# Kernel optimization log

Measured on AMD Instinct MI355X. Metric: run time of the kernel, lower is better.

The kernel has to match this reference:

```python
import jax, jax.numpy as jnp
from jax import lax
import numpy as np

DIM = 64
NUM_HEADS = 1
SR_RATIO = 8
LN_EPS = 1e-3  # Keras LayerNormalization default


def setup_inputs() -> dict:
    key = jax.random.key(0)
    ks = jax.random.split(key, 8)
    B, H, W = 8, 128, 128
    N, C = H * W, DIM
    s = 0.02
    x = jax.random.normal(ks[0], (B, N, C), dtype=jnp.float32)
    Wq = jax.random.normal(ks[1], (C, C), dtype=jnp.float32) * s
    Wkv = jax.random.normal(ks[2], (C, 2 * C), dtype=jnp.float32) * s
    sr_kernel = jax.random.normal(ks[3], (SR_RATIO, SR_RATIO, C, C), dtype=jnp.float32) * s
    sr_bias = jnp.zeros((C,), dtype=jnp.float32)
    ln_gamma = jnp.ones((C,), dtype=jnp.float32)
    ln_beta = jnp.zeros((C,), dtype=jnp.float32)
    Wproj = jax.random.normal(ks[4], (C, C), dtype=jnp.float32) * s
    bproj = jnp.zeros((C,), dtype=jnp.float32)
    return {"x": x, "H": H, "W": W, "Wq": Wq, "Wkv": Wkv,
            "sr_kernel": sr_kernel, "sr_bias": sr_bias,
            "ln_gamma": ln_gamma, "ln_beta": ln_beta,
            "Wproj": Wproj, "bproj": bproj}


def reference(x, H, W, Wq, Wkv, sr_kernel, sr_bias, ln_gamma, ln_beta, Wproj, bproj):
    B, N, C = x.shape
    nh = NUM_HEADS
    hd = C // nh
    scale = hd ** -0.5

    # q: [B, nh, N, hd]
    q = (x @ Wq).reshape(B, N, nh, hd).transpose(0, 2, 1, 3)

    # spatial-reduction KV path (faithful to the TF code, incl. its
    # transpose-then-reshape ordering)
    x_ = jnp.transpose(x, (0, 2, 1)).reshape(B, H, W, C)
    x_ = lax.conv_general_dilated(
        x_, sr_kernel, window_strides=(SR_RATIO, SR_RATIO), padding="VALID",
        dimension_numbers=("NHWC", "HWIO", "NHWC")) + sr_bias
    M = x_.shape[1] * x_.shape[2]
    x_ = x_.reshape(B, M, C)
    # LayerNorm over last axis
    mu = jnp.mean(x_, axis=-1, keepdims=True)
    var = jnp.mean(jnp.square(x_ - mu), axis=-1, keepdims=True)
    x_ = (x_ - mu) * lax.rsqrt(var + LN_EPS) * ln_gamma + ln_beta

    kv = (x_ @ Wkv).reshape(B, M, 2, nh, hd).transpose(2, 0, 3, 1, 4)
    k, v = kv[0], kv[1]  # [B, nh, M, hd]

    attn = jax.nn.softmax(jnp.einsum("bhnd,bhmd->bhnm", q, k) * scale, axis=-1)
    out = jnp.einsum("bhnm,bhmd->bhnd", attn, v)
    out = out.transpose(0, 2, 1, 3).reshape(B, N, C)
    return out @ Wproj + bproj
```

## Files before the change

### kernel.cpp

```cpp
#include <hip/hip_runtime.h>
#include <hip/hip_bf16.h>

#define B_   8
#define N_   16384
#define C_   64
#define M_   256
#define NPB  1048576

typedef __attribute__((ext_vector_type(8))) short short8v;
typedef __attribute__((ext_vector_type(16))) float f32x16;
typedef __attribute__((ext_vector_type(4)))  float f32x4;

union FragU { short8v s8; unsigned u[4]; };

__device__ inline unsigned pkbf(float a, float b) {
  union { __hip_bfloat162 h2; unsigned u; } cv;
  cv.h2 = __float22bfloat162_rn(make_float2(a, b));
  return cv.u;
}
__device__ inline unsigned short bfbits(float a) {
  union { __hip_bfloat16 h; unsigned short u; } cv;
  cv.h = __float2bfloat16(a);
  return cv.u;
}
__device__ inline float bf2f(unsigned short u) {
  union { unsigned u; float f; } cv;
  cv.u = ((unsigned)u) << 16;
  return cv.f;
}
__device__ inline short8v ld8(const unsigned short* p) {
  return *(const short8v*)p;
}

__device__ inline void plswap(unsigned &a, unsigned &b) {
#if __has_builtin(__builtin_amdgcn_permlane32_swap)
  typedef unsigned uint2v __attribute__((ext_vector_type(2)));
  uint2v r = __builtin_amdgcn_permlane32_swap(a, b, false, false);
  a = r[0]; b = r[1];
#else
  asm volatile("v_permlane32_swap_b32 %0, %1" : "+v"(a), "+v"(b));
#endif
}

__device__ inline void repack16(const f32x16 s, FragU& f0, FragU& f1) {
  #pragma unroll
  for (int h = 0; h < 2; ++h) {
    FragU& f = h ? f1 : f0;
    unsigned a0 = pkbf(s[8*h+0], s[8*h+1]);
    unsigned a1 = pkbf(s[8*h+2], s[8*h+3]);
    unsigned a2 = pkbf(s[8*h+4], s[8*h+5]);
    unsigned a3 = pkbf(s[8*h+6], s[8*h+7]);
    plswap(a0, a2);
    plswap(a1, a3);
    f.u[0] = a0; f.u[1] = a1; f.u[2] = a2; f.u[3] = a3;
  }
}

__global__ __launch_bounds__(256) void prep(const float* __restrict__ Wq,
                                            const float* __restrict__ Wp,
                                            const float* __restrict__ Kw,
                                            const float* __restrict__ Wkv,
                                            unsigned short* __restrict__ kbt,
                                            float* __restrict__ wkp,
                                            float* __restrict__ wvp) {
  const int gi = blockIdx.x;
  if (gi < 1024) {
    const int idx = gi * 256 + threadIdx.x;
    const int j = idx & 7, l = (idx >> 3) & 63, s = (idx >> 9) & 15;
    const int w = (idx >> 13) & 3, kw = idx >> 15;
    const int e = s * 32 + 8 * (l >> 4) + j;
    const int par = e >> 8, ci = (e >> 2) & 63, jj = e & 3;
    const int kh = 2 * jj + par, co = 16 * w + (l & 15);
    kbt[idx] = bfbits(Kw[(size_t)((kh * 8 + kw) * 64 + ci) * 64 + co]);
  } else {
    const int idx = (gi - 1024) * 256 + threadIdx.x;
    const int c = idx & 63, cc = (idx >> 6) & 63, sel = idx >> 12;
    float s = 0.f;
    if (sel == 0) {
      #pragma unroll 8
      for (int d = 0; d < 64; ++d) s += Wkv[cc * 128 + d] * Wq[c * 64 + d];
      wkp[cc * 64 + c] = s * 0.125f;
    } else {
      #pragma unroll 8
      for (int d = 0; d < 64; ++d) s += Wkv[cc * 128 + 64 + d] * Wp[d * 64 + c];
      wvp[cc * 64 + c] = s;
    }
  }
}

__global__ __launch_bounds__(256) void conv_mfma(const float* __restrict__ x,
                                                 const unsigned short* __restrict__ kbt,
                                                 unsigned short* __restrict__ xrb) {
  const int kw = blockIdx.x & 7;
  const int ow = (blockIdx.x >> 3) & 15;
  const int b  = blockIdx.x >> 7;
  const int t  = threadIdx.x, w = t >> 6, l = t & 63;
  const int oh = l & 15, kg = l >> 4;

  const float* xb = x + (size_t)b * NPB + (size_t)((ow * 8 + kw) * 64) * 64 + oh * 4;
  const unsigned short* kb = kbt + (size_t)(((kw * 4 + w) * 16) * 64 + l) * 8;

  f32x4 acc = {0.f, 0.f, 0.f, 0.f};
  #pragma unroll
  for (int s = 0; s < 16; ++s) {
    const int par = (s >= 8) ? 1 : 0;
    const int ci  = ((s * 8) + kg * 2) & 63;
    const float* ax = xb + (size_t)par * 524288 + ci * 64;
    const float4 a0 = *(const float4*)(ax);
    const float4 a1 = *(const float4*)(ax + 64);
    FragU af;
    af.u[0] = pkbf(a0.x, a0.y); af.u[1] = pkbf(a0.z, a0.w);
    af.u[2] = pkbf(a1.x, a1.y); af.u[3] = pkbf(a1.z, a1.w);
    const short8v bfrag = ld8(kb + s * 512);
    acc = __builtin_amdgcn_mfma_f32_16x16x32_bf16(af.s8, bfrag, acc, 0, 0, 0);
  }
  unsigned short* dst = xrb + (size_t)kw * 131072
                      + ((size_t)b * 256 + ow) * 64 + w * 16 + (l & 15);
  #pragma unroll
  for (int r = 0; r < 4; ++r)
    dst[(size_t)((l >> 4) * 4 + r) * 1024] = bfbits(acc[r]);
}

__global__ __launch_bounds__(256) void ln_kv(const unsigned short* __restrict__ xrb,
                                             const float* __restrict__ sr_bias,
                                             const float* __restrict__ gamma,
                                             const float* __restrict__ beta,
                                             const float* __restrict__ wkp,
                                             const float* __restrict__ wvp,
                                             unsigned short* __restrict__ kbl,
                                             unsigned short* __restrict__ vbl) {
  const int w   = threadIdx.x >> 6;
  const int row = blockIdx.x * 4 + w;
  const int c   = threadIdx.x & 63;
  float val = sr_bias[c];
  #pragma unroll
  for (int s = 0; s < 8; ++s)
    val += bf2f(xrb[(size_t)s * 131072 + (size_t)row * 64 + c]);

  float sum = val;
  #pragma unroll
  for (int off = 32; off; off >>= 1) sum += __shfl_xor(sum, off, 64);
  const float mu = sum * (1.f / 64.f);
  const float d  = val - mu;
  float vs = d * d;
  #pragma unroll
  for (int off = 32; off; off >>= 1) vs += __shfl_xor(vs, off, 64);
  const float rs = rsqrtf(vs * (1.f / 64.f) + 1e-3f);
  const float ln = d * rs * gamma[c] + beta[c];

  __shared__ float lnrow[4][64];
  lnrow[w][c] = ln;
  __syncthreads();

  float ka = 0.f, va = 0.f;
  #pragma unroll 8
  for (int cc = 0; cc < 64; ++cc) {
    const float l = lnrow[w][cc];
    ka += l * wkp[cc * 64 + c];
    va += l * wvp[cc * 64 + c];
  }
  const int m = row & 255, bb = row >> 8;
  kbl[(size_t)bb * 16384
      + (size_t)((((m >> 5) * 4 + (c >> 4)) * 64) + (m & 31) + 32 * ((c >> 3) & 1)) * 8
      + (c & 7)] = bfbits(ka);
  vbl[(size_t)bb * 16384
      + (size_t)(((c >> 5) * 8 + (m >> 5)) * 2 + ((m >> 4) & 1)) * 512
      + (size_t)((c & 31) + 32 * ((m >> 3) & 1)) * 8
      + (m & 7)] = bfbits(va);
}

__global__ __launch_bounds__(256, 4) void attn_mfma(const float* __restrict__ x,
                                                    const unsigned short* __restrict__ kbl,
                                                    const unsigned short* __restrict__ vbl,
                                                    const float* __restrict__ bp,
                                                    float* __restrict__ out) {
  __shared__ float ot[128 * 68];
  const int t    = threadIdx.x;
  const int w    = t >> 6;
  const int l    = t & 63;
  const int l31  = l & 31;
  const int hi   = l >> 5;
  const int b    = blockIdx.x >> 7;
  const int tile = blockIdx.x & 127;
  const size_t nrow = (size_t)b * N_ + (size_t)tile * 128;
  const int qrow = w * 32 + l31;

  const float* xrow = x + (nrow + qrow) * 64;
  FragU xb[4];
  #pragma unroll
  for (int tt = 0; tt < 4; ++tt) {
    const float* p = xrow + 16 * tt + 8 * hi;
    const float4 x0 = *(const float4*)(p);
    const float4 x1 = *(const float4*)(p + 4);
    xb[tt].u[0] = pkbf(x0.x, x0.y); xb[tt].u[1] = pkbf(x0.z, x0.w);
    xb[tt].u[2] = pkbf(x1.x, x1.y); xb[tt].u[3] = pkbf(x1.z, x1.w);
  }

  const unsigned short* kfp = kbl + (size_t)b * 16384 + l * 8;
  const unsigned short* vfp = vbl + (size_t)b * 16384 + l * 8;
  f32x16 O0, O1;
  #pragma unroll
  for (int r = 0; r < 16; ++r) { O0[r] = 0.f; O1[r] = 0.f; }
  float ss = 0.f;

  #pragma unroll
  for (int kt = 0; kt < 8; ++kt) {
    const short8v vf00 = ld8(vfp + (size_t)((kt * 2 + 0) * 512));
    const short8v vf01 = ld8(vfp + (size_t)((kt * 2 + 1) * 512));
    const short8v vf10 = ld8(vfp + (size_t)(((8 + kt) * 2 + 0) * 512));
    const short8v vf11 = ld8(vfp + (size_t)(((8 + kt) * 2 + 1) * 512));
    f32x16 S;
    #pragma unroll
    for (int r = 0; r < 16; ++r) S[r] = 0.f;
    #pragma unroll
    for (int tt = 0; tt < 4; ++tt) {
      const short8v ak = ld8(kfp + (size_t)((kt * 4 + tt) * 512));
      S = __builtin_amdgcn_mfma_f32_32x32x16_bf16(ak, xb[tt].s8, S, 0, 0, 0);
    }
    f32x16 P;
    #pragma unroll
    for (int r = 0; r < 16; ++r) {
      const float pv = __expf(S[r]);
      P[r] = pv; ss += pv;
    }
    FragU f0, f1;
    repack16(P, f0, f1);
    O0 = __builtin_amdgcn_mfma_f32_32x32x16_bf16(vf00, f0.s8, O0, 0, 0, 0);
    O0 = __builtin_amdgcn_mfma_f32_32x32x16_bf16(vf01, f1.s8, O0, 0, 0, 0);
    O1 = __builtin_amdgcn_mfma_f32_32x32x16_bf16(vf10, f0.s8, O1, 0, 0, 0);
    O1 = __builtin_amdgcn_mfma_f32_32x32x16_bf16(vf11, f1.s8, O1, 0, 0, 0);
  }

  ss += __shfl_xor(ss, 32);
  const float inv = 1.f / ss;
  #pragma unroll
  for (int g = 0; g < 4; ++g) {
    {
      const int co = 8 * g + 4 * hi;
      const float4 bb = *(const float4*)(bp + co);
      *(float4*)&ot[qrow * 68 + co] =
          make_float4(O0[4 * g + 0] * inv + bb.x, O0[4 * g + 1] * inv + bb.y,
                      O0[4 * g + 2] * inv + bb.z, O0[4 * g + 3] * inv + bb.w);
    }
    {
      const int co = 32 + 8 * g + 4 * hi;
      const float4 bb = *(const float4*)(bp + co);
      *(float4*)&ot[qrow * 68 + co] =
          make_float4(O1[4 * g + 0] * inv + bb.x, O1[4 * g + 1] * inv + bb.y,
                      O1[4 * g + 2] * inv + bb.z, O1[4 * g + 3] * inv + bb.w);
    }
  }

  __syncthreads();
  float4* out4 = (float4*)(out + nrow * 64);
  #pragma unroll
  for (int i = 0; i < 8; ++i) {
    const int idx = i * 256 + t;
    const int row = idx >> 4, c4 = idx & 15;
    out4[idx] = *(const float4*)&ot[row * 68 + c4 * 4];
  }
}

extern "C" void kernel_launch(void* const* d_in, const int* in_sizes, int n_in,
                              void* d_out, int out_size, void* d_ws, size_t ws_size,
                              hipStream_t stream) {
  const float* x   = (const float*)d_in[0];
  const float* Wq  = (const float*)d_in[3];
  const float* Wkv = (const float*)d_in[4];
  const float* Kw  = (const float*)d_in[5];
  const float* sb  = (const float*)d_in[6];
  const float* gam = (const float*)d_in[7];
  const float* bet = (const float*)d_in[8];
  const float* Wp  = (const float*)d_in[9];
  const float* bp  = (const float*)d_in[10];
  float* out = (float*)d_out;

  unsigned short* xrb = (unsigned short*)d_ws;
  unsigned short* kbl = xrb + 1048576;
  unsigned short* vbl = kbl + 131072;
  unsigned short* kbt = vbl + 131072;
  float* wkp = (float*)(kbt + 262144);
  float* wvp = wkp + 4096;

  prep<<<1056, 256, 0, stream>>>(Wq, Wp, Kw, Wkv, kbt, wkp, wvp);
  conv_mfma<<<1024, 256, 0, stream>>>(x, kbt, xrb);
  ln_kv<<<512, 256, 0, stream>>>(xrb, sb, gam, bet, wkp, wvp, kbl, vbl);
  attn_mfma<<<1024, 256, 0, stream>>>(x, kbl, vbl, bp, out);
}
```

Before: 46.85 us.

## Process two query tiles per wave to reuse K/V fragments, use exp2

Each wave of the attention kernel now handles 64 query rows as two 32-row sub-tiles, so every loaded K and V fragment feeds twice as many MFMAs and the block count halves. The log2(e) factor is folded into the precomputed key weight so softmax can use exp2f instead of __expf. Launch bounds drop to 2 blocks per CU to make room for the doubled accumulator registers, and the output is written in two passes through the same shared tile with extra barriers. The cost is fewer resident waves per CU and more synchronisation in the epilogue.

```diff
diff --git a/kernel.cpp b/kernel.cpp
--- a/kernel.cpp
+++ b/kernel.cpp
@@ -79,7 +79,7 @@
     if (sel == 0) {
       #pragma unroll 8
       for (int d = 0; d < 64; ++d) s += Wkv[cc * 128 + d] * Wq[c * 64 + d];
-      wkp[cc * 64 + c] = s * 0.125f;
+      wkp[cc * 64 + c] = s * 0.125f * 1.4426950408889634f;
     } else {
       #pragma unroll 8
       for (int d = 0; d < 64; ++d) s += Wkv[cc * 128 + 64 + d] * Wp[d * 64 + c];
@@ -169,7 +169,7 @@
       + (m & 7)] = bfbits(va);
 }
 
-__global__ __launch_bounds__(256, 4) void attn_mfma(const float* __restrict__ x,
+__global__ __launch_bounds__(256, 2) void attn_mfma(const float* __restrict__ x,
                                                     const unsigned short* __restrict__ kbl,
                                                     const unsigned short* __restrict__ vbl,
                                                     const float* __restrict__ bp,
@@ -180,28 +180,34 @@
   const int l    = t & 63;
   const int l31  = l & 31;
   const int hi   = l >> 5;
-  const int b    = blockIdx.x >> 7;
-  const int tile = blockIdx.x & 127;
-  const size_t nrow = (size_t)b * N_ + (size_t)tile * 128;
-  const int qrow = w * 32 + l31;
-
-  const float* xrow = x + (nrow + qrow) * 64;
-  FragU xb[4];
+  const int b    = blockIdx.x >> 6;
+  const int tile = blockIdx.x & 63;
+  const size_t nrow = (size_t)b * N_ + (size_t)tile * 256;
+  const int qA = w * 64 + l31;
+
+  const float* xrowA = x + (nrow + qA) * 64;
+  FragU xa[4], xbb[4];
   #pragma unroll
   for (int tt = 0; tt < 4; ++tt) {
-    const float* p = xrow + 16 * tt + 8 * hi;
-    const float4 x0 = *(const float4*)(p);
-    const float4 x1 = *(const float4*)(p + 4);
-    xb[tt].u[0] = pkbf(x0.x, x0.y); xb[tt].u[1] = pkbf(x0.z, x0.w);
-    xb[tt].u[2] = pkbf(x1.x, x1.y); xb[tt].u[3] = pkbf(x1.z, x1.w);
+    const float* pA = xrowA + 16 * tt + 8 * hi;
+    const float4 a0 = *(const float4*)(pA);
+    const float4 a1 = *(const float4*)(pA + 4);
+    xa[tt].u[0] = pkbf(a0.x, a0.y); xa[tt].u[1] = pkbf(a0.z, a0.w);
+    xa[tt].u[2] = pkbf(a1.x, a1.y); xa[tt].u[3] = pkbf(a1.z, a1.w);
+    const float* pB = pA + 32 * 64;
+    const float4 b0 = *(const float4*)(pB);
+    const float4 b1 = *(const float4*)(pB + 4);
+    xbb[tt].u[0] = pkbf(b0.x, b0.y); xbb[tt].u[1] = pkbf(b0.z, b0.w);
+    xbb[tt].u[2] = pkbf(b1.x, b1.y); xbb[tt].u[3] = pkbf(b1.z, b1.w);
   }
 
   const unsigned short* kfp = kbl + (size_t)b * 16384 + l * 8;
   const unsigned short* vfp = vbl + (size_t)b * 16384 + l * 8;
-  f32x16 O0, O1;
-  #pragma unroll
-  for (int r = 0; r < 16; ++r) { O0[r] = 0.f; O1[r] = 0.f; }
-  float ss = 0.f;
+  f32x16 Z;
+  #pragma unroll
+  for (int r = 0; r < 16; ++r) Z[r] = 0.f;
+  f32x16 OA0 = Z, OA1 = Z, OB0 = Z, OB1 = Z;
+  float ssA = 0.f, ssB = 0.f;
 
   #pragma unroll
   for (int kt = 0; kt < 8; ++kt) {
@@ -209,55 +215,88 @@
     const short8v vf01 = ld8(vfp + (size_t)((kt * 2 + 1) * 512));
     const short8v vf10 = ld8(vfp + (size_t)(((8 + kt) * 2 + 0) * 512));
     const short8v vf11 = ld8(vfp + (size_t)(((8 + kt) * 2 + 1) * 512));
-    f32x16 S;
-    #pragma unroll
-    for (int r = 0; r < 16; ++r) S[r] = 0.f;
-    #pragma unroll
-    for (int tt = 0; tt < 4; ++tt) {
-      const short8v ak = ld8(kfp + (size_t)((kt * 4 + tt) * 512));
-      S = __builtin_amdgcn_mfma_f32_32x32x16_bf16(ak, xb[tt].s8, S, 0, 0, 0);
-    }
-    f32x16 P;
+    const short8v ak0 = ld8(kfp + (size_t)((kt * 4 + 0) * 512));
+    const short8v ak1 = ld8(kfp + (size_t)((kt * 4 + 1) * 512));
+    const short8v ak2 = ld8(kfp + (size_t)((kt * 4 + 2) * 512));
+    const short8v ak3 = ld8(kfp + (size_t)((kt * 4 + 3) * 512));
+    f32x16 Sa = __builtin_amdgcn_mfma_f32_32x32x16_bf16(ak0, xa[0].s8, Z, 0, 0, 0);
+    f32x16 Sb = __builtin_amdgcn_mfma_f32_32x32x16_bf16(ak0, xbb[0].s8, Z, 0, 0, 0);
+    Sa = __builtin_amdgcn_mfma_f32_32x32x16_bf16(ak1, xa[1].s8, Sa, 0, 0, 0);
+    Sb = __builtin_amdgcn_mfma_f32_32x32x16_bf16(ak1, xbb[1].s8, Sb, 0, 0, 0);
+    Sa = __builtin_amdgcn_mfma_f32_32x32x16_bf16(ak2, xa[2].s8, Sa, 0, 0, 0);
+    Sb = __builtin_amdgcn_mfma_f32_32x32x16_bf16(ak2, xbb[2].s8, Sb, 0, 0, 0);
+    Sa = __builtin_amdgcn_mfma_f32_32x32x16_bf16(ak3, xa[3].s8, Sa, 0, 0, 0);
+    Sb = __builtin_amdgcn_mfma_f32_32x32x16_bf16(ak3, xbb[3].s8, Sb, 0, 0, 0);
+    f32x16 Pa, Pb;
     #pragma unroll
     for (int r = 0; r < 16; ++r) {
-      const float pv = __expf(S[r]);
-      P[r] = pv; ss += pv;
+      const float pa = exp2f(Sa[r]);  Pa[r] = pa; ssA += pa;
+      const float pb = exp2f(Sb[r]);  Pb[r] = pb; ssB += pb;
     }
-    FragU f0, f1;
-    repack16(P, f0, f1);
-    O0 = __builtin_amdgcn_mfma_f32_32x32x16_bf16(vf00, f0.s8, O0, 0, 0, 0);
-    O0 = __builtin_amdgcn_mfma_f32_32x32x16_bf16(vf01, f1.s8, O0, 0, 0, 0);
-    O1 = __builtin_amdgcn_mfma_f32_32x32x16_bf16(vf10, f0.s8, O1, 0, 0, 0);
-    O1 = __builtin_amdgcn_mfma_f32_32x32x16_bf16(vf11, f1.s8, O1, 0, 0, 0);
-  }
-
-  ss += __shfl_xor(ss, 32);
-  const float inv = 1.f / ss;
+    FragU fa0, fa1, fb0, fb1;
+    repack16(Pa, fa0, fa1);
+    repack16(Pb, fb0, fb1);
+    OA0 = __builtin_amdgcn_mfma_f32_32x32x16_bf16(vf00, fa0.s8, OA0, 0, 0, 0);
+    OB0 = __builtin_amdgcn_mfma_f32_32x32x16_bf16(vf00, fb0.s8, OB0, 0, 0, 0);
+    OA1 = __builtin_amdgcn_mfma_f32_32x32x16_bf16(vf10, fa0.s8, OA1, 0, 0, 0);
+    OB1 = __builtin_amdgcn_mfma_f32_32x32x16_bf16(vf10, fb0.s8, OB1, 0, 0, 0);
+    OA0 = __builtin_amdgcn_mfma_f32_32x32x16_bf16(vf01, fa1.s8, OA0, 0, 0, 0);
+    OB0 = __builtin_amdgcn_mfma_f32_32x32x16_bf16(vf01, fb1.s8, OB0, 0, 0, 0);
+    OA1 = __builtin_amdgcn_mfma_f32_32x32x16_bf16(vf11, fa1.s8, OA1, 0, 0, 0);
+    OB1 = __builtin_amdgcn_mfma_f32_32x32x16_bf16(vf11, fb1.s8, OB1, 0, 0, 0);
+  }
+
+  ssA += __shfl_xor(ssA, 32);
+  ssB += __shfl_xor(ssB, 32);
+  const float invA = 1.f / ssA, invB = 1.f / ssB;
+  const int slot = w * 32 + l31;
+
   #pragma unroll
   for (int g = 0; g < 4; ++g) {
-    {
-      const int co = 8 * g + 4 * hi;
-      const float4 bb = *(const float4*)(bp + co);
-      *(float4*)&ot[qrow * 68 + co] =
-          make_float4(O0[4 * g + 0] * inv + bb.x, O0[4 * g + 1] * inv + bb.y,
-                      O0[4 * g + 2] * inv + bb.z, O0[4 * g + 3] * inv + bb.w);
+    const int co0 = 8 * g + 4 * hi, co1 = 32 + 8 * g + 4 * hi;
+    const float4 b0 = *(const float4*)(bp + co0);
+    const float4 b1 = *(const float4*)(bp + co1);
+    *(float4*)&ot[slot * 68 + co0] =
+        make_float4(OA0[4*g+0]*invA + b0.x, OA0[4*g+1]*invA + b0.y,
+                    OA0[4*g+2]*invA + b0.z, OA0[4*g+3]*invA + b0.w);
+    *(float4*)&ot[slot * 68 + co1] =
+        make_float4(OA1[4*g+0]*invA + b1.x, OA1[4*g+1]*invA + b1.y,
+                    OA1[4*g+2]*invA + b1.z, OA1[4*g+3]*invA + b1.w);
+  }
+  __syncthreads();
+  {
+    #pragma unroll
+    for (int i = 0; i < 8; ++i) {
+      const int idx = i * 256 + t;
+      const int s = idx >> 4, c4 = idx & 15;
+      const int wp = s >> 5, r = s & 31;
+      *(float4*)(out + (nrow + wp * 64 + r) * 64 + c4 * 4) =
+          *(const float4*)&ot[s * 68 + c4 * 4];
     }
-    {
-      const int co = 32 + 8 * g + 4 * hi;
-      const float4 bb = *(const float4*)(bp + co);
-      *(float4*)&ot[qrow * 68 + co] =
-          make_float4(O1[4 * g + 0] * inv + bb.x, O1[4 * g + 1] * inv + bb.y,
-                      O1[4 * g + 2] * inv + bb.z, O1[4 * g + 3] * inv + bb.w);
+  }
+  __syncthreads();
+  #pragma unroll
+  for (int g = 0; g < 4; ++g) {
+    const int co0 = 8 * g + 4 * hi, co1 = 32 + 8 * g + 4 * hi;
+    const float4 b0 = *(const float4*)(bp + co0);
+    const float4 b1 = *(const float4*)(bp + co1);
+    *(float4*)&ot[slot * 68 + co0] =
+        make_float4(OB0[4*g+0]*invB + b0.x, OB0[4*g+1]*invB + b0.y,
+                    OB0[4*g+2]*invB + b0.z, OB0[4*g+3]*invB + b0.w);
+    *(float4*)&ot[slot * 68 + co1] =
+        make_float4(OB1[4*g+0]*invB + b1.x, OB1[4*g+1]*invB + b1.y,
+                    OB1[4*g+2]*invB + b1.z, OB1[4*g+3]*invB + b1.w);
+  }
+  __syncthreads();
+  {
+    #pragma unroll
+    for (int i = 0; i < 8; ++i) {
+      const int idx = i * 256 + t;
+      const int s = idx >> 4, c4 = idx & 15;
+      const int wp = s >> 5, r = s & 31;
+      *(float4*)(out + (nrow + wp * 64 + 32 + r) * 64 + c4 * 4) =
+          *(const float4*)&ot[s * 68 + c4 * 4];
     }
-  }
-
-  __syncthreads();
-  float4* out4 = (float4*)(out + nrow * 64);
-  #pragma unroll
-  for (int i = 0; i < 8; ++i) {
-    const int idx = i * 256 + t;
-    const int row = idx >> 4, c4 = idx & 15;
-    out4[idx] = *(const float4*)&ot[row * 68 + c4 * 4];
   }
 }
 
@@ -285,5 +324,5 @@
   prep<<<1056, 256, 0, stream>>>(Wq, Wp, Kw, Wkv, kbt, wkp, wvp);
   conv_mfma<<<1024, 256, 0, stream>>>(x, kbt, xrb);
   ln_kv<<<512, 256, 0, stream>>>(xrb, sb, gam, bet, wkp, wvp, kbl, vbl);
-  attn_mfma<<<1024, 256, 0, stream>>>(x, kbl, vbl, bp, out);
-}
+  attn_mfma<<<512, 256, 0, stream>>>(x, kbl, vbl, bp, out);
+}
```

Result: slower. 49.39 us (+5.4%).

## Stage K/V in LDS with 512-thread attention blocks and exp2 softmax

Applied to the files above, without the earlier changes.

The attention kernel now uses 512-thread blocks covering 256 query rows. Each block cooperatively copies the per-batch K and V fragments (64 KB) into shared memory, and the MFMA loop reads them from there instead of global memory. The log2(e) factor is folded into the precomputed K weights so the softmax can use exp2f, and the first MFMA takes a zero accumulator directly. The output staging reuses the same LDS in two phases. The costs are 64 KB of LDS per block, which limits occupancy, plus an extra barrier and copy before compute.

```diff
diff --git a/kernel.cpp b/kernel.cpp
--- a/kernel.cpp
+++ b/kernel.cpp
@@ -79,7 +79,7 @@
     if (sel == 0) {
       #pragma unroll 8
       for (int d = 0; d < 64; ++d) s += Wkv[cc * 128 + d] * Wq[c * 64 + d];
-      wkp[cc * 64 + c] = s * 0.125f;
+      wkp[cc * 64 + c] = s * 0.125f * 1.4426950408889634f;
     } else {
       #pragma unroll 8
       for (int d = 0; d < 64; ++d) s += Wkv[cc * 128 + 64 + d] * Wp[d * 64 + c];
@@ -169,23 +169,38 @@
       + (m & 7)] = bfbits(va);
 }
 
-__global__ __launch_bounds__(256, 4) void attn_mfma(const float* __restrict__ x,
+__global__ __launch_bounds__(512, 4) void attn_mfma(const float* __restrict__ x,
                                                     const unsigned short* __restrict__ kbl,
                                                     const unsigned short* __restrict__ vbl,
                                                     const float* __restrict__ bp,
                                                     float* __restrict__ out) {
-  __shared__ float ot[128 * 68];
+  __shared__ char smem[65536];
+  unsigned short* ks = (unsigned short*)smem;
+  unsigned short* vs = ks + 16384;
   const int t    = threadIdx.x;
   const int w    = t >> 6;
   const int l    = t & 63;
   const int l31  = l & 31;
   const int hi   = l >> 5;
-  const int b    = blockIdx.x >> 7;
-  const int tile = blockIdx.x & 127;
-  const size_t nrow = (size_t)b * N_ + (size_t)tile * 128;
-  const int qrow = w * 32 + l31;
-
-  const float* xrow = x + (nrow + qrow) * 64;
+  const int b    = blockIdx.x >> 6;
+  const int tile = blockIdx.x & 63;
+  const size_t nrow = (size_t)b * N_ + (size_t)tile * 256;
+  const int qloc = w * 32 + l31;
+
+  {
+    typedef __attribute__((ext_vector_type(2))) unsigned long long ull2;
+    const ull2* kg = (const ull2*)(kbl + (size_t)b * 16384);
+    const ull2* vg = (const ull2*)(vbl + (size_t)b * 16384);
+    ull2* kd = (ull2*)ks;
+    ull2* vd = (ull2*)vs;
+    #pragma unroll
+    for (int i = 0; i < 4; ++i) {
+      kd[i * 512 + t] = kg[i * 512 + t];
+      vd[i * 512 + t] = vg[i * 512 + t];
+    }
+  }
+
+  const float* xrow = x + (nrow + qloc) * 64;
   FragU xb[4];
   #pragma unroll
   for (int tt = 0; tt < 4; ++tt) {
@@ -195,12 +210,14 @@
     xb[tt].u[0] = pkbf(x0.x, x0.y); xb[tt].u[1] = pkbf(x0.z, x0.w);
     xb[tt].u[2] = pkbf(x1.x, x1.y); xb[tt].u[3] = pkbf(x1.z, x1.w);
   }
-
-  const unsigned short* kfp = kbl + (size_t)b * 16384 + l * 8;
-  const unsigned short* vfp = vbl + (size_t)b * 16384 + l * 8;
-  f32x16 O0, O1;
-  #pragma unroll
-  for (int r = 0; r < 16; ++r) { O0[r] = 0.f; O1[r] = 0.f; }
+  __syncthreads();
+
+  const unsigned short* kfp = ks + l * 8;
+  const unsigned short* vfp = vs + l * 8;
+  f32x16 Z;
+  #pragma unroll
+  for (int r = 0; r < 16; ++r) Z[r] = 0.f;
+  f32x16 O0 = Z, O1 = Z;
   float ss = 0.f;
 
   #pragma unroll
@@ -209,18 +226,17 @@
     const short8v vf01 = ld8(vfp + (size_t)((kt * 2 + 1) * 512));
     const short8v vf10 = ld8(vfp + (size_t)(((8 + kt) * 2 + 0) * 512));
     const short8v vf11 = ld8(vfp + (size_t)(((8 + kt) * 2 + 1) * 512));
-    f32x16 S;
+    f32x16 S = __builtin_amdgcn_mfma_f32_32x32x16_bf16(
+        ld8(kfp + (size_t)((kt * 4 + 0) * 512)), xb[0].s8, Z, 0, 0, 0);
     #pragma unroll
-    for (int r = 0; r < 16; ++r) S[r] = 0.f;
-    #pragma unroll
-    for (int tt = 0; tt < 4; ++tt) {
+    for (int tt = 1; tt < 4; ++tt) {
       const short8v ak = ld8(kfp + (size_t)((kt * 4 + tt) * 512));
       S = __builtin_amdgcn_mfma_f32_32x32x16_bf16(ak, xb[tt].s8, S, 0, 0, 0);
     }
     f32x16 P;
     #pragma unroll
     for (int r = 0; r < 16; ++r) {
-      const float pv = __expf(S[r]);
+      const float pv = exp2f(S[r]);
       P[r] = pv; ss += pv;
     }
     FragU f0, f1;
@@ -233,31 +249,36 @@
 
   ss += __shfl_xor(ss, 32);
   const float inv = 1.f / ss;
-  #pragma unroll
-  for (int g = 0; g < 4; ++g) {
-    {
-      const int co = 8 * g + 4 * hi;
-      const float4 bb = *(const float4*)(bp + co);
-      *(float4*)&ot[qrow * 68 + co] =
-          make_float4(O0[4 * g + 0] * inv + bb.x, O0[4 * g + 1] * inv + bb.y,
-                      O0[4 * g + 2] * inv + bb.z, O0[4 * g + 3] * inv + bb.w);
-    }
-    {
-      const int co = 32 + 8 * g + 4 * hi;
-      const float4 bb = *(const float4*)(bp + co);
-      *(float4*)&ot[qrow * 68 + co] =
-          make_float4(O1[4 * g + 0] * inv + bb.x, O1[4 * g + 1] * inv + bb.y,
-                      O1[4 * g + 2] * inv + bb.z, O1[4 * g + 3] * inv + bb.w);
-    }
-  }
-
+
+  float* ot = (float*)smem;
   __syncthreads();
-  float4* out4 = (float4*)(out + nrow * 64);
-  #pragma unroll
-  for (int i = 0; i < 8; ++i) {
-    const int idx = i * 256 + t;
-    const int row = idx >> 4, c4 = idx & 15;
-    out4[idx] = *(const float4*)&ot[row * 68 + c4 * 4];
+
+  #pragma unroll
+  for (int ph = 0; ph < 2; ++ph) {
+    if ((w >> 2) == ph) {
+      const int slot = (w & 3) * 32 + l31;
+      #pragma unroll
+      for (int g = 0; g < 4; ++g) {
+        const int co0 = 8 * g + 4 * hi, co1 = 32 + 8 * g + 4 * hi;
+        const float4 b0 = *(const float4*)(bp + co0);
+        const float4 b1 = *(const float4*)(bp + co1);
+        *(float4*)&ot[slot * 68 + co0] =
+            make_float4(O0[4*g+0]*inv + b0.x, O0[4*g+1]*inv + b0.y,
+                        O0[4*g+2]*inv + b0.z, O0[4*g+3]*inv + b0.w);
+        *(float4*)&ot[slot * 68 + co1] =
+            make_float4(O1[4*g+0]*inv + b1.x, O1[4*g+1]*inv + b1.y,
+                        O1[4*g+2]*inv + b1.z, O1[4*g+3]*inv + b1.w);
+      }
+    }
+    __syncthreads();
+    float4* out4 = (float4*)(out + (nrow + ph * 128) * 64);
+    #pragma unroll
+    for (int i = 0; i < 4; ++i) {
+      const int idx = i * 512 + t;
+      const int row = idx >> 4, c4 = idx & 15;
+      out4[idx] = *(const float4*)&ot[row * 68 + c4 * 4];
+    }
+    __syncthreads();
   }
 }
 
@@ -285,5 +306,5 @@
   prep<<<1056, 256, 0, stream>>>(Wq, Wp, Kw, Wkv, kbt, wkp, wvp);
   conv_mfma<<<1024, 256, 0, stream>>>(x, kbt, xrb);
   ln_kv<<<512, 256, 0, stream>>>(xrb, sb, gam, bet, wkp, wvp, kbl, vbl);
-  attn_mfma<<<1024, 256, 0, stream>>>(x, kbl, vbl, bp, out);
-}
+  attn_mfma<<<512, 512, 0, stream>>>(x, kbl, vbl, bp, out);
+}
```

After: 47.86 us. +2.2%, slower.
